# Kernel tuning notes

Hardware: AMD Instinct MI355X
Metric: run time of the kernel (lower is better)

The kernel has to match this reference:

```python
import jax, jax.numpy as jnp
import numpy as np

N, E, D, H, ED = 50000, 800000, 128, 16, 16
TAU = 0.5

def _seg_sum(data, ids, n):
    return jax.ops.segment_sum(data, ids, num_segments=n)

def gcn_conv(x, src, dst, ew, W, b, n):
    # PyG-style GCNConv with added self-loops (weight 1) and symmetric normalization
    xw = x @ W                                   # [n, out]
    deg = _seg_sum(ew, dst, n) + 1.0             # in-degree incl. self-loop
    dinv = jax.lax.rsqrt(deg)
    norm = dinv[src] * ew * dinv[dst]            # [E]
    out = _seg_sum(xw[src] * norm[:, None], dst, n)
    out = out + xw * (dinv * dinv)[:, None]      # self-loop message
    return out + b

def layer_norm(x, g, b, eps=1e-5):
    mu = jnp.mean(x, -1, keepdims=True)
    var = jnp.mean((x - mu) ** 2, -1, keepdims=True)
    return (x - mu) * jax.lax.rsqrt(var + eps) * g + b

def gumbel_hard(logits, u, tau):
    # F.gumbel_softmax(hard=True) with straight-through estimator
    g = -jnp.log(-jnp.log(u + 1e-10) + 1e-10)
    y = jax.nn.softmax((logits + g) / tau, axis=-1)
    hard = jax.nn.one_hot(jnp.argmax(y, -1), y.shape[-1], dtype=y.dtype)
    return hard + y - jax.lax.stop_gradient(y)

def action_net(x, src, dst, w1, b1, w2, b2, n):
    ones = jnp.ones((src.shape[0],), x.dtype)
    h = jax.nn.relu(gcn_conv(x, src, dst, ones, w1, b1, n))
    return gcn_conv(h, src, dst, ones, w2, b2, n)    # [n, 2]

def setup_inputs():
    key = jax.random.key(0)
    ks = jax.random.split(key, 12)
    p = lambda k, s: (0.02 * jax.random.normal(k, s)).astype(jnp.float32)
    return dict(
        x=jax.random.normal(ks[0], (N, D), jnp.float32),
        edge_index=jax.random.randint(ks[1], (2, E), 0, N, jnp.int32),
        edge_attr=jax.random.normal(ks[2], (E, ED), jnp.float32),
        u_in=jax.random.uniform(ks[3], (N, 2), jnp.float32),
        u_out=jax.random.uniform(ks[4], (N, 2), jnp.float32),
        ln_g=jnp.ones((D,), jnp.float32), ln_b=jnp.zeros((D,), jnp.float32),
        conv_w=p(ks[5], (D, D)), conv_b=jnp.zeros((D,), jnp.float32),
        ep_w=p(ks[6], (ED, D)), ep_b=jnp.zeros((D,), jnp.float32),
        ia1_w=p(ks[7], (D, H)), ia1_b=jnp.zeros((H,), jnp.float32),
        ia2_w=p(ks[8], (H, 2)), ia2_b=jnp.zeros((2,), jnp.float32),
        oa1_w=p(ks[9], (D, H)), oa1_b=jnp.zeros((H,), jnp.float32),
        oa2_w=p(ks[10], (H, 2)), oa2_b=jnp.zeros((2,), jnp.float32),
    )

def reference(x, edge_index, edge_attr, u_in, u_out, ln_g, ln_b, conv_w, conv_b,
              ep_w, ep_b, ia1_w, ia1_b, ia2_w, ia2_b, oa1_w, oa1_b, oa2_w, oa2_b):
    src, dst = edge_index[0], edge_index[1]
    # edge_proj (dropout is identity in eval mode)
    edge_features = jax.nn.relu(edge_attr @ ep_w + ep_b)      # [E, D]
    xn = layer_norm(x, ln_g, ln_b)
    in_logits = action_net(xn, src, dst, ia1_w, ia1_b, ia2_w, ia2_b, N)
    out_logits = action_net(xn, src, dst, oa1_w, oa1_b, oa2_w, oa2_b, N)
    in_probs = gumbel_hard(in_logits, u_in, TAU)
    out_probs = gumbel_hard(out_logits, u_out, TAU)
    edge_weight = in_probs[dst, 0] * out_probs[src, 0]        # [E]
    out = gcn_conv(xn, src, dst, edge_weight, conv_w, conv_b, N)
    out = out + _seg_sum(edge_features, dst, N)
    return jax.nn.relu(out)
```

## Files before the change

kernel.cpp:

```cpp
#include <hip/hip_runtime.h>
#include <hip/hip_bf16.h>

#define DD 128
#define HH 16
#define SCAN_B 1024
#define EPB 256
#define VT_STRIDE 132

typedef __bf16 bf16x8 __attribute__((ext_vector_type(8)));
typedef float f32x4 __attribute__((ext_vector_type(4)));

__global__ void ln_kernel(const float* __restrict__ x, const float* __restrict__ g,
                          const float* __restrict__ b, float* __restrict__ xn, int n_nodes) {
  int w = (blockIdx.x * blockDim.x + threadIdx.x) >> 6;
  int lane = threadIdx.x & 63;
  if (w >= n_nodes) return;
  const float* xr = x + (size_t)w * DD;
  float a0 = xr[lane], a1 = xr[lane + 64];
  float s = a0 + a1;
  #pragma unroll
  for (int o = 32; o > 0; o >>= 1) s += __shfl_down(s, o);
  s = __shfl(s, 0);
  float mu = s * (1.0f / DD);
  float d0 = a0 - mu, d1 = a1 - mu;
  float v = d0 * d0 + d1 * d1;
  #pragma unroll
  for (int o = 32; o > 0; o >>= 1) v += __shfl_down(v, o);
  v = __shfl(v, 0);
  float rstd = rsqrtf(v * (1.0f / DD) + 1e-5f);
  float* xo = xn + (size_t)w * DD;
  xo[lane]      = d0 * rstd * g[lane] + b[lane];
  xo[lane + 64] = d1 * rstd * g[lane + 64] + b[lane + 64];
}

__global__ __launch_bounds__(256) void proj1_kernel(const float* __restrict__ xn,
    const float* __restrict__ ia1_w, const float* __restrict__ oa1_w,
    float* __restrict__ xw_a, int n_nodes) {
  __shared__ __align__(16) float wl[DD * 32];
  for (int i = threadIdx.x; i < DD * HH; i += 256) {
    int dd = i >> 4, jj = i & 15;
    wl[dd * 32 + jj]      = ia1_w[i];
    wl[dd * 32 + 16 + jj] = oa1_w[i];
  }
  __syncthreads();
  int t = blockIdx.x * blockDim.x + threadIdx.x;
  int n = t >> 5, j = t & 31;
  if (n >= n_nodes) return;
  const float* xr = xn + (size_t)n * DD;
  float acc = 0.f;
  #pragma unroll 8
  for (int d = 0; d < DD; ++d) acc = fmaf(xr[d], wl[d * 32 + j], acc);
  xw_a[(size_t)n * 32 + j] = acc;
}

__global__ void degcnt_kernel(const int* __restrict__ dst, int* __restrict__ deg, int n_edges) {
  int e = blockIdx.x * blockDim.x + threadIdx.x;
  if (e < n_edges) atomicAdd(&deg[dst[e]], 1);
}

__global__ __launch_bounds__(SCAN_B) void scan1_kernel(const int* __restrict__ deg,
    int* __restrict__ rs, int* __restrict__ partials, int n_nodes) {
  __shared__ int sm[SCAN_B];
  int i = blockIdx.x * SCAN_B + threadIdx.x;
  int v = (i < n_nodes) ? deg[i] : 0;
  sm[threadIdx.x] = v;
  __syncthreads();
  for (int o = 1; o < SCAN_B; o <<= 1) {
    int t = (threadIdx.x >= o) ? sm[threadIdx.x - o] : 0;
    __syncthreads();
    sm[threadIdx.x] += t;
    __syncthreads();
  }
  if (i < n_nodes) rs[i] = sm[threadIdx.x] - v;
  if (threadIdx.x == SCAN_B - 1) partials[blockIdx.x] = sm[threadIdx.x];
}

__global__ __launch_bounds__(SCAN_B) void scan2_kernel(int* __restrict__ partials, int nb) {
  __shared__ int sm[SCAN_B];
  int v = (threadIdx.x < nb) ? partials[threadIdx.x] : 0;
  sm[threadIdx.x] = v;
  __syncthreads();
  for (int o = 1; o < SCAN_B; o <<= 1) {
    int t = (threadIdx.x >= o) ? sm[threadIdx.x - o] : 0;
    __syncthreads();
    sm[threadIdx.x] += t;
    __syncthreads();
  }
  if (threadIdx.x < nb) partials[threadIdx.x] = sm[threadIdx.x] - v;
}

__global__ __launch_bounds__(SCAN_B) void scan3_kernel(int* __restrict__ rs,
    const int* __restrict__ partials, int n_nodes) {
  int i = blockIdx.x * SCAN_B + threadIdx.x;
  if (i < n_nodes) rs[i] += partials[blockIdx.x];
}

__global__ void fill_kernel(const int* __restrict__ src, const int* __restrict__ dst,
    int* __restrict__ rs, int* __restrict__ csr_eid, int* __restrict__ csr_src, int n_edges) {
  int e = blockIdx.x * blockDim.x + threadIdx.x;
  if (e >= n_edges) return;
  int d = dst[e];
  int pos = atomicAdd(&rs[d], 1);
  csr_eid[pos] = e;
  csr_src[pos] = src[e];
}

__global__ void dinva_kernel(const int* __restrict__ deg, float* __restrict__ dinv, int n_nodes) {
  int i = blockIdx.x * blockDim.x + threadIdx.x;
  if (i < n_nodes) dinv[i] = rsqrtf((float)deg[i] + 1.0f);
}

__global__ __launch_bounds__(256) void agg1_kernel(const int* __restrict__ rs,
    const int* __restrict__ deg, const int* __restrict__ csr_src,
    const float* __restrict__ xw_a, const float* __restrict__ dinva,
    const float* __restrict__ ia1_b, const float* __restrict__ oa1_b,
    const float* __restrict__ ia2_w, const float* __restrict__ oa2_w,
    float* __restrict__ xw2_a, int n_nodes) {
  int t = blockIdx.x * blockDim.x + threadIdx.x;
  int node = t >> 5, j = t & 31;
  if (node >= n_nodes) return;
  int dg = deg[node];
  int st = rs[node] - dg;
  float acc = 0.f;
  for (int i = 0; i < dg; ++i) {
    int s = csr_src[st + i];
    acc = fmaf(xw_a[(size_t)s * 32 + j], dinva[s], acc);
  }
  float di = dinva[node];
  float bias = (j < 16) ? ia1_b[j] : oa1_b[j - 16];
  float h = fmaxf(acc * di + xw_a[(size_t)node * 32 + j] * di * di + bias, 0.f);
  float w0 = (j < 16) ? ia2_w[j * 2 + 0] : oa2_w[(j - 16) * 2 + 0];
  float w1 = (j < 16) ? ia2_w[j * 2 + 1] : oa2_w[(j - 16) * 2 + 1];
  float p0 = h * w0, p1 = h * w1;
  #pragma unroll
  for (int o = 1; o < 16; o <<= 1) { p0 += __shfl_xor(p0, o); p1 += __shfl_xor(p1, o); }
  if ((j & 15) == 0) {
    int k = j >> 4;
    xw2_a[(size_t)node * 4 + k * 2 + 0] = p0;
    xw2_a[(size_t)node * 4 + k * 2 + 1] = p1;
  }
}

__global__ void agg2_kernel(const int* __restrict__ rs, const int* __restrict__ deg,
    const int* __restrict__ csr_src, const float* __restrict__ xw2_a,
    const float* __restrict__ dinva, const float* __restrict__ ia2_b,
    const float* __restrict__ oa2_b, const float* __restrict__ u_in,
    const float* __restrict__ u_out, float* __restrict__ fin, float* __restrict__ fout,
    int n_nodes) {
  int t = blockIdx.x * blockDim.x + threadIdx.x;
  int node = t >> 4, l = t & 15;
  if (node >= n_nodes) return;
  int dg = deg[node];
  int st = rs[node] - dg;
  float a0 = 0.f, a1 = 0.f, a2 = 0.f, a3 = 0.f;
  for (int i = l; i < dg; i += 16) {
    int s = csr_src[st + i];
    float ds = dinva[s];
    float4 v = *(const float4*)&xw2_a[(size_t)s * 4];
    a0 = fmaf(v.x, ds, a0); a1 = fmaf(v.y, ds, a1);
    a2 = fmaf(v.z, ds, a2); a3 = fmaf(v.w, ds, a3);
  }
  #pragma unroll
  for (int o = 1; o < 16; o <<= 1) {
    a0 += __shfl_xor(a0, o); a1 += __shfl_xor(a1, o);
    a2 += __shfl_xor(a2, o); a3 += __shfl_xor(a3, o);
  }
  if (l == 0) {
    float di = dinva[node], sw = di * di;
    float4 self = *(const float4*)&xw2_a[(size_t)node * 4];
    float li0 = a0 * di + self.x * sw + ia2_b[0];
    float li1 = a1 * di + self.y * sw + ia2_b[1];
    float lo0 = a2 * di + self.z * sw + oa2_b[0];
    float lo1 = a3 * di + self.w * sw + oa2_b[1];
    float gi0 = -logf(-logf(u_in[(size_t)node * 2 + 0] + 1e-10f) + 1e-10f);
    float gi1 = -logf(-logf(u_in[(size_t)node * 2 + 1] + 1e-10f) + 1e-10f);
    float go0 = -logf(-logf(u_out[(size_t)node * 2 + 0] + 1e-10f) + 1e-10f);
    float go1 = -logf(-logf(u_out[(size_t)node * 2 + 1] + 1e-10f) + 1e-10f);
    fin[node]  = (li0 + gi0 >= li1 + gi1) ? 1.f : 0.f;
    fout[node] = (lo0 + go0 >= lo1 + go1) ? 1.f : 0.f;
  }
}

__global__ void cdeg_kernel(const int* __restrict__ rs, const int* __restrict__ deg,
    const int* __restrict__ csr_src, const float* __restrict__ fin,
    const float* __restrict__ fout, float* __restrict__ dinvc, int n_nodes) {
  int t = blockIdx.x * blockDim.x + threadIdx.x;
  int node = t >> 4, l = t & 15;
  if (node >= n_nodes) return;
  int dg = deg[node];
  int st = rs[node] - dg;
  float c = 0.f;
  if (fin[node] != 0.f) {
    for (int i = l; i < dg; i += 16) c += (fout[csr_src[st + i]] != 0.f) ? 1.f : 0.f;
  }
  #pragma unroll
  for (int o = 1; o < 16; o <<= 1) c += __shfl_xor(c, o);
  if (l == 0) dinvc[node] = rsqrtf(c + 1.0f);
}

#define GEMM_ROWS 64
__global__ __launch_bounds__(256) void gemm_kernel(const float* __restrict__ xn,
    const float* __restrict__ W, float* __restrict__ xwc, int n_nodes) {
  __shared__ __align__(16) float wl[DD * DD];
  for (int i = threadIdx.x * 4; i < DD * DD; i += 256 * 4)
    *(float4*)&wl[i] = *(const float4*)&W[i];
  __syncthreads();
  int c4 = (threadIdx.x & 31) * 4;
  int r0 = threadIdx.x >> 5;
  int base = blockIdx.x * GEMM_ROWS;
  for (int r = r0; r < GEMM_ROWS; r += 8) {
    int n = base + r;
    if (n >= n_nodes) break;
    const float* xr = xn + (size_t)n * DD;
    float4 acc = {0.f, 0.f, 0.f, 0.f};
    #pragma unroll 4
    for (int d = 0; d < DD; ++d) {
      float xv = xr[d];
      float4 w = *(const float4*)&wl[d * DD + c4];
      acc.x = fmaf(xv, w.x, acc.x);
      acc.y = fmaf(xv, w.y, acc.y);
      acc.z = fmaf(xv, w.z, acc.z);
      acc.w = fmaf(xv, w.w, acc.w);
    }
    *(float4*)&xwc[(size_t)n * DD + c4] = acc;
  }
}

__global__ __launch_bounds__(256) void edgenode_kernel(
    const int* __restrict__ rs, const int* __restrict__ deg,
    const int* __restrict__ csr_src, const int* __restrict__ csr_eid,
    const float* __restrict__ ea, const float* __restrict__ ep_w,
    const float* __restrict__ ep_b, const float* __restrict__ xwc,
    const float* __restrict__ dinvc, const float* __restrict__ fin,
    const float* __restrict__ fout, float* __restrict__ out_acc,
    int n_nodes, int n_edges) {
  __shared__ __align__(16) __bf16 vt[EPB * VT_STRIDE];
  __shared__ float comb[2][DD];
  const int tid = threadIdx.x;
  const int P = blockIdx.x * EPB;
  const int Pend = min(P + EPB, n_edges);

  {
    const int l = tid & 63;
    const int w = tid >> 6;
    const int col = l & 15;
    const int kg = l >> 4;
    const int k0 = kg * 8;
    bf16x8 bfr[8];
    float bias[8];
    #pragma unroll
    for (int nt = 0; nt < 8; ++nt) {
      int j = nt * 16 + col;
      bf16x8 bb = {};
      if (k0 < HH) {
        #pragma unroll
        for (int i = 0; i < 8; ++i) bb[i] = (__bf16)ep_w[(k0 + i) * DD + j];
      }
      bfr[nt] = bb;
      bias[nt] = ep_b[j];
    }
    #pragma unroll
    for (int t = 0; t < 4; ++t) {
      int tile = w * 4 + t;
      int pos0 = P + tile * 16;
      if (pos0 < n_edges) {
        int apos = pos0 + col;
        int eid = csr_eid[(apos < n_edges) ? apos : (n_edges - 1)];
        bf16x8 afr = {};
        if (k0 < HH) {
          const float4* er = (const float4*)(ea + (size_t)eid * HH + k0);
          float4 f0 = er[0], f1 = er[1];
          afr[0] = (__bf16)f0.x; afr[1] = (__bf16)f0.y;
          afr[2] = (__bf16)f0.z; afr[3] = (__bf16)f0.w;
          afr[4] = (__bf16)f1.x; afr[5] = (__bf16)f1.y;
          afr[6] = (__bf16)f1.z; afr[7] = (__bf16)f1.w;
        }
        #pragma unroll
        for (int nt = 0; nt < 8; ++nt) {
          f32x4 d4 = {0.f, 0.f, 0.f, 0.f};
          d4 = __builtin_amdgcn_mfma_f32_16x16x32_bf16(afr, bfr[nt], d4, 0, 0, 0);
          #pragma unroll
          for (int r = 0; r < 4; ++r) {
            int rowl = tile * 16 + kg * 4 + r;
            vt[rowl * VT_STRIDE + nt * 16 + col] = (__bf16)fmaxf(d4[r] + bias[nt], 0.f);
          }
        }
      }
    }
  }
  __syncthreads();

  const int j = tid & 127;
  const int h = tid >> 7;
  int lo = 0, hi = n_nodes;
  while (lo < hi) {
    int mid = (lo + hi) >> 1;
    if (rs[mid] > P) hi = mid; else lo = mid + 1;
  }
  int d = lo;
  int p = P;
  int seg = 0;
  while (p < Pend) {
    int re = rs[d];
    if (re <= p) { ++d; continue; }
    int se = (re < Pend) ? re : Pend;
    float fd = fin[d] * dinvc[d];
    float sum = 0.f;
    int pstart = p + (((p & 1) == h) ? 0 : 1);
    if (fd != 0.f) {
      for (int p2 = pstart; p2 < se; p2 += 2) {
        sum += (float)vt[(p2 - P) * VT_STRIDE + j];
        int s = csr_src[p2];
        float fs = fout[s];
        if (fs != 0.f) sum = fmaf(fd * dinvc[s], xwc[(size_t)s * DD + j], sum);
      }
    } else {
      for (int p2 = pstart; p2 < se; p2 += 2)
        sum += (float)vt[(p2 - P) * VT_STRIDE + j];
    }
    int k = seg & 1;
    if (h == 1) comb[k][j] = sum;
    __syncthreads();
    if (h == 0) {
      float total = sum + comb[k][j];
      bool full = (se == re) && (p == re - deg[d]);
      if (full) out_acc[(size_t)d * DD + j] = total;
      else atomicAdd(&out_acc[(size_t)d * DD + j], total);
    }
    p = se;
    if (se == re) ++d;
    ++seg;
  }
}

__global__ void final_kernel(float* __restrict__ out_acc, const float* __restrict__ xwc,
    const float* __restrict__ dinvc, const float* __restrict__ conv_b, int n_nodes) {
  int t = blockIdx.x * blockDim.x + threadIdx.x;
  if (t >= n_nodes * DD) return;
  int n = t >> 7, j = t & 127;
  float di = dinvc[n];
  float v = out_acc[t] + xwc[t] * di * di + conv_b[j];
  out_acc[t] = fmaxf(v, 0.f);
}

extern "C" void kernel_launch(void* const* d_in, const int* in_sizes, int n_in,
                              void* d_out, int out_size, void* d_ws, size_t ws_size,
                              hipStream_t stream) {
  const float* x      = (const float*)d_in[0];
  const int*   eidx   = (const int*)d_in[1];
  const float* ea     = (const float*)d_in[2];
  const float* u_in   = (const float*)d_in[3];
  const float* u_out  = (const float*)d_in[4];
  const float* ln_g   = (const float*)d_in[5];
  const float* ln_b   = (const float*)d_in[6];
  const float* conv_w = (const float*)d_in[7];
  const float* conv_b = (const float*)d_in[8];
  const float* ep_w   = (const float*)d_in[9];
  const float* ep_b   = (const float*)d_in[10];
  const float* ia1_w  = (const float*)d_in[11];
  const float* ia1_b  = (const float*)d_in[12];
  const float* ia2_w  = (const float*)d_in[13];
  const float* ia2_b  = (const float*)d_in[14];
  const float* oa1_w  = (const float*)d_in[15];
  const float* oa1_b  = (const float*)d_in[16];
  const float* oa2_w  = (const float*)d_in[17];
  const float* oa2_b  = (const float*)d_in[18];

  const int n = in_sizes[0] / DD;
  const int E = in_sizes[1] / 2;
  const int* src = eidx;
  const int* dst = eidx + E;

  float* ws = (float*)d_ws;
  float* xn    = ws;
  float* xw_a  = xn + (size_t)n * 128;
  float* xw2_a = xw_a + (size_t)n * 32;
  float* dinva = xw2_a + (size_t)n * 4;
  float* xwc   = dinva + n;
  int* deg_i   = (int*)(xwc + (size_t)n * 128);
  int* rs      = deg_i + n;
  int* partials= rs + n;
  int* csr_eid = partials + 1024;
  int* csr_src = csr_eid + E;
  float* fin   = xw_a;
  float* fout  = xw_a + n;
  float* dinvc = xw_a + 2 * (size_t)n;

  float* out_acc = (float*)d_out;

  hipMemsetAsync(deg_i, 0, (size_t)n * sizeof(int), stream);
  hipMemsetAsync(d_out, 0, (size_t)out_size * sizeof(float), stream);

  const int B = 256;
  const int nb = (n + SCAN_B - 1) / SCAN_B;

  ln_kernel<<<(n * 64 + B - 1) / B, B, 0, stream>>>(x, ln_g, ln_b, xn, n);
  proj1_kernel<<<(n * 32 + B - 1) / B, B, 0, stream>>>(xn, ia1_w, oa1_w, xw_a, n);
  degcnt_kernel<<<(E + B - 1) / B, B, 0, stream>>>(dst, deg_i, E);
  scan1_kernel<<<nb, SCAN_B, 0, stream>>>(deg_i, rs, partials, n);
  scan2_kernel<<<1, SCAN_B, 0, stream>>>(partials, nb);
  scan3_kernel<<<nb, SCAN_B, 0, stream>>>(rs, partials, n);
  dinva_kernel<<<(n + B - 1) / B, B, 0, stream>>>(deg_i, dinva, n);
  fill_kernel<<<(E + B - 1) / B, B, 0, stream>>>(src, dst, rs, csr_eid, csr_src, E);
  agg1_kernel<<<(n * 32 + B - 1) / B, B, 0, stream>>>(rs, deg_i, csr_src, xw_a, dinva,
                                                      ia1_b, oa1_b, ia2_w, oa2_w, xw2_a, n);
  agg2_kernel<<<(n * 16 + B - 1) / B, B, 0, stream>>>(rs, deg_i, csr_src, xw2_a, dinva,
                                                      ia2_b, oa2_b, u_in, u_out, fin, fout, n);
  cdeg_kernel<<<(n * 16 + B - 1) / B, B, 0, stream>>>(rs, deg_i, csr_src, fin, fout, dinvc, n);
  gemm_kernel<<<(n + GEMM_ROWS - 1) / GEMM_ROWS, B, 0, stream>>>(xn, conv_w, xwc, n);
  edgenode_kernel<<<(E + EPB - 1) / EPB, B, 0, stream>>>(rs, deg_i, csr_src, csr_eid,
      ea, ep_w, ep_b, xwc, dinvc, fin, fout, out_acc, n, E);
  final_kernel<<<((size_t)n * DD + B - 1) / B, B, 0, stream>>>(out_acc, xwc, dinvc, conv_b, n);
}
```

Baseline: 786.1 us.

## Restructure edgenode aggregation into per-wave segments, halve edges per block, fuse dinva

The edge-node kernel now processes 128 edges per block instead of 256. Each edge position binary-searches its destination node, and a ballot-based compaction builds a shared-memory list of destination segments. Each wave then owns whole segments and handles two columns per lane with float2 loads and bf16 unpacking, removing the per-segment __syncthreads and the half-block combine step. The dinva computation is also folded into scan3, saving one launch. In exchange there are twice as many blocks (more MFMA weight setup and more boundary atomics), a per-thread binary search, and idle waves when a block has few segments.

```diff
diff --git a/kernel.cpp b/kernel.cpp
--- a/kernel.cpp
+++ b/kernel.cpp
@@ -4,7 +4,7 @@
 #define DD 128
 #define HH 16
 #define SCAN_B 1024
-#define EPB 256
+#define EPB 128
 #define VT_STRIDE 132
 
 typedef __bf16 bf16x8 __attribute__((ext_vector_type(8)));
@@ -90,9 +90,13 @@
 }
 
 __global__ __launch_bounds__(SCAN_B) void scan3_kernel(int* __restrict__ rs,
-    const int* __restrict__ partials, int n_nodes) {
+    const int* __restrict__ partials, const int* __restrict__ deg,
+    float* __restrict__ dinva, int n_nodes) {
   int i = blockIdx.x * SCAN_B + threadIdx.x;
-  if (i < n_nodes) rs[i] += partials[blockIdx.x];
+  if (i < n_nodes) {
+    rs[i] += partials[blockIdx.x];
+    dinva[i] = rsqrtf((float)deg[i] + 1.0f);
+  }
 }
 
 __global__ void fill_kernel(const int* __restrict__ src, const int* __restrict__ dst,
@@ -103,11 +107,6 @@
   int pos = atomicAdd(&rs[d], 1);
   csr_eid[pos] = e;
   csr_src[pos] = src[e];
-}
-
-__global__ void dinva_kernel(const int* __restrict__ deg, float* __restrict__ dinv, int n_nodes) {
-  int i = blockIdx.x * blockDim.x + threadIdx.x;
-  if (i < n_nodes) dinv[i] = rsqrtf((float)deg[i] + 1.0f);
 }
 
 __global__ __launch_bounds__(256) void agg1_kernel(const int* __restrict__ rs,
@@ -235,7 +234,10 @@
     const float* __restrict__ fout, float* __restrict__ out_acc,
     int n_nodes, int n_edges) {
   __shared__ __align__(16) __bf16 vt[EPB * VT_STRIDE];
-  __shared__ float comb[2][DD];
+  __shared__ int dpos[EPB];
+  __shared__ int seg_start[EPB + 1];
+  __shared__ int seg_d[EPB];
+  __shared__ int wcnt[2];
   const int tid = threadIdx.x;
   const int P = blockIdx.x * EPB;
   const int Pend = min(P + EPB, n_edges);
@@ -260,8 +262,8 @@
       bias[nt] = ep_b[j];
     }
     #pragma unroll
-    for (int t = 0; t < 4; ++t) {
-      int tile = w * 4 + t;
+    for (int t = 0; t < 2; ++t) {
+      int tile = w * 2 + t;
       int pos0 = P + tile * 16;
       if (pos0 < n_edges) {
         int apos = pos0 + col;
@@ -288,48 +290,81 @@
       }
     }
   }
-  __syncthreads();
-
-  const int j = tid & 127;
-  const int h = tid >> 7;
-  int lo = 0, hi = n_nodes;
-  while (lo < hi) {
-    int mid = (lo + hi) >> 1;
-    if (rs[mid] > P) hi = mid; else lo = mid + 1;
-  }
-  int d = lo;
-  int p = P;
-  int seg = 0;
-  while (p < Pend) {
-    int re = rs[d];
-    if (re <= p) { ++d; continue; }
-    int se = (re < Pend) ? re : Pend;
+
+  if (tid < EPB) {
+    int pos = P + tid;
+    int d = -1;
+    if (pos < n_edges) {
+      int lo = 0, hi = n_nodes;
+      while (lo < hi) {
+        int mid = (lo + hi) >> 1;
+        if (rs[mid] > pos) hi = mid; else lo = mid + 1;
+      }
+      d = lo;
+    }
+    dpos[tid] = d;
+  }
+  __syncthreads();
+
+  bool flag = false;
+  if (tid < EPB && (P + tid) < n_edges)
+    flag = (tid == 0) || (dpos[tid] != dpos[tid - 1]);
+  unsigned long long bm = 0;
+  int pre = 0;
+  if (tid < EPB) {
+    bm = __ballot(flag);
+    int lane = tid & 63;
+    pre = __popcll(bm & ((1ull << lane) - 1));
+    if (lane == 0) wcnt[tid >> 6] = __popcll(bm);
+  }
+  __syncthreads();
+  int NSEG = wcnt[0] + wcnt[1];
+  if (flag) {
+    int idx = pre + ((tid >> 6) ? wcnt[0] : 0);
+    seg_start[idx] = tid;
+    seg_d[idx] = dpos[tid];
+  }
+  if (tid == 0) seg_start[NSEG] = Pend - P;
+  __syncthreads();
+
+  const int wid = tid >> 6;
+  const int l = tid & 63;
+  for (int sg = wid; sg < NSEG; sg += 4) {
+    int p0 = seg_start[sg];
+    int p1 = seg_start[sg + 1];
+    int d = seg_d[sg];
     float fd = fin[d] * dinvc[d];
-    float sum = 0.f;
-    int pstart = p + (((p & 1) == h) ? 0 : 1);
+    float s0 = 0.f, s1 = 0.f;
     if (fd != 0.f) {
-      for (int p2 = pstart; p2 < se; p2 += 2) {
-        sum += (float)vt[(p2 - P) * VT_STRIDE + j];
-        int s = csr_src[p2];
+      for (int p = p0; p < p1; ++p) {
+        unsigned u = *(const unsigned*)&vt[p * VT_STRIDE + 2 * l];
+        s0 += __uint_as_float(u << 16);
+        s1 += __uint_as_float(u & 0xffff0000u);
+        int s = csr_src[P + p];
         float fs = fout[s];
-        if (fs != 0.f) sum = fmaf(fd * dinvc[s], xwc[(size_t)s * DD + j], sum);
+        if (fs != 0.f) {
+          float2 w = *(const float2*)(xwc + (size_t)s * DD + 2 * l);
+          float c = fd * dinvc[s];
+          s0 = fmaf(w.x, c, s0);
+          s1 = fmaf(w.y, c, s1);
+        }
       }
     } else {
-      for (int p2 = pstart; p2 < se; p2 += 2)
-        sum += (float)vt[(p2 - P) * VT_STRIDE + j];
-    }
-    int k = seg & 1;
-    if (h == 1) comb[k][j] = sum;
-    __syncthreads();
-    if (h == 0) {
-      float total = sum + comb[k][j];
-      bool full = (se == re) && (p == re - deg[d]);
-      if (full) out_acc[(size_t)d * DD + j] = total;
-      else atomicAdd(&out_acc[(size_t)d * DD + j], total);
-    }
-    p = se;
-    if (se == re) ++d;
-    ++seg;
+      for (int p = p0; p < p1; ++p) {
+        unsigned u = *(const unsigned*)&vt[p * VT_STRIDE + 2 * l];
+        s0 += __uint_as_float(u << 16);
+        s1 += __uint_as_float(u & 0xffff0000u);
+      }
+    }
+    int gend = rs[d];
+    bool full = ((P + p0) == gend - deg[d]) && ((P + p1) == gend);
+    if (full) {
+      float2 res = {s0, s1};
+      *(float2*)(out_acc + (size_t)d * DD + 2 * l) = res;
+    } else {
+      atomicAdd(&out_acc[(size_t)d * DD + 2 * l], s0);
+      atomicAdd(&out_acc[(size_t)d * DD + 2 * l + 1], s1);
+    }
   }
 }
 
@@ -399,8 +434,7 @@
   degcnt_kernel<<<(E + B - 1) / B, B, 0, stream>>>(dst, deg_i, E);
   scan1_kernel<<<nb, SCAN_B, 0, stream>>>(deg_i, rs, partials, n);
   scan2_kernel<<<1, SCAN_B, 0, stream>>>(partials, nb);
-  scan3_kernel<<<nb, SCAN_B, 0, stream>>>(rs, partials, n);
-  dinva_kernel<<<(n + B - 1) / B, B, 0, stream>>>(deg_i, dinva, n);
+  scan3_kernel<<<nb, SCAN_B, 0, stream>>>(rs, partials, deg_i, dinva, n);
   fill_kernel<<<(E + B - 1) / B, B, 0, stream>>>(src, dst, rs, csr_eid, csr_src, E);
   agg1_kernel<<<(n * 32 + B - 1) / B, B, 0, stream>>>(rs, deg_i, csr_src, xw_a, dinva,
                                                       ia1_b, oa1_b, ia2_w, oa2_w, xw2_a, n);
```

Measured after the change: 645.5 us. 1.22x faster.
